# Optimization experiments

Measured on AMD Instinct MI355X. Metric: run time of the kernel, lower is better.

The kernel has to match this reference:

```python
import jax, jax.numpy as jnp
import numpy as np

EPS = 1e-5

def conv2d(x, w, stride=1, pad=0, groups=1):
    return jax.lax.conv_general_dilated(
        x, w, (stride, stride), [(pad, pad), (pad, pad)],
        feature_group_count=groups,
        dimension_numbers=('NCHW', 'OIHW', 'NCHW'))

def prelu(x, a):
    return jnp.where(x > 0, x, a[None, :, None, None] * x)

def batchnorm(x, g, b):
    # training-mode BN: batch statistics over N,H,W (biased variance, as torch)
    m = jnp.mean(x, axis=(0, 2, 3), keepdims=True)
    v = jnp.var(x, axis=(0, 2, 3), keepdims=True)
    xhat = (x - m) * jax.lax.rsqrt(v + EPS)
    return xhat * g[None, :, None, None] + b[None, :, None, None]

def setup_inputs() -> dict:
    key = jax.random.key(0)
    ks = jax.random.split(key, 8)
    C_in, C_out, stride = 128, 256, 2
    x = jax.random.normal(ks[0], (32, C_in, 56, 56), dtype=jnp.float32)
    w1 = jax.random.normal(ks[1], (C_out, C_in, 1, 1), dtype=jnp.float32) * 0.05
    w_dw = jax.random.normal(ks[2], (C_out, 1, 3, 3), dtype=jnp.float32) * 0.1
    w3 = jax.random.normal(ks[3], (C_out, C_out, 1, 1), dtype=jnp.float32) * 0.05
    w_adj = jax.random.normal(ks[4], (C_out, C_in, 1, 1), dtype=jnp.float32) * 0.05
    a_init = jnp.full((C_out,), 0.25, dtype=jnp.float32)  # PReLU init
    ones = jnp.ones((C_out,), dtype=jnp.float32)
    zeros = jnp.zeros((C_out,), dtype=jnp.float32)
    return {
        'x': x,
        'w1': w1, 'a1': a_init, 'g1': ones, 'b1': zeros,
        'w_dw': w_dw, 'a2': a_init, 'g2': ones, 'b2': zeros,
        'w3': w3, 'a3': a_init, 'g3': ones, 'b3': zeros,
        'w_adj': w_adj,
    }

def reference(x, w1, a1, g1, b1, w_dw, a2, g2, b2, w3, a3, g3, b3, w_adj):
    stride, C_out = 2, w_dw.shape[0]
    residual = conv2d(x, w_adj, stride=stride)  # full-precision shortcut
    xs = jnp.sign(x)
    # binary 1x1 conv (sign(x) already signed; sign is idempotent)
    out = conv2d(jnp.sign(xs), jnp.sign(w1))
    out = batchnorm(prelu(out, a1), g1, b1)
    # binary depthwise 3x3, stride, pad 1
    out = conv2d(jnp.sign(out), jnp.sign(w_dw), stride=stride, pad=1, groups=C_out)
    out = batchnorm(prelu(out, a2), g2, b2)
    # binary 1x1 conv
    out = conv2d(jnp.sign(out), jnp.sign(w3))
    out = batchnorm(prelu(out, a3), g3, b3)
    return out + residual
```

## Files before the change

### kernel.cpp

```cpp
#include <hip/hip_runtime.h>
#include <stdint.h>

#define NB   32
#define CIN  128
#define COUT 256
#define HH   56
#define WW   56
#define S1   (HH*WW)
#define HO   28
#define WO   28
#define S2   (HO*WO)
#define NS1  (NB*S1)
#define NS2  (NB*S2)
#define TOT2 (NS2*COUT)
#define EPSV 1e-5f

constexpr size_t OFF_XBITS = 0;
constexpr size_t OFF_WB1   = OFF_XBITS + (size_t)NS1*8*4;
constexpr size_t OFF_WB3   = OFF_WB1 + 256*8*4;
constexpr size_t OFF_WDW   = OFF_WB3 + 256*16*4;
constexpr size_t OFF_ACC   = OFF_WDW + 4096;
constexpr size_t OFF_WBADJ = OFF_ACC + 3*256*4*sizeof(int);
constexpr size_t OFF_XG    = OFF_WBADJ + (size_t)COUT*CIN*2;
constexpr size_t OFF_OUT1  = OFF_XG + (size_t)NS2*CIN*2;
constexpr size_t OFF_OUT2  = OFF_OUT1 + (size_t)NS1*COUT;
constexpr size_t OFF_XB2   = OFF_OUT2 + (size_t)TOT2;
constexpr size_t OFF_OUT3  = OFF_XB2 + (size_t)NS2*16*4;

typedef __attribute__((ext_vector_type(8))) short bf16x8;
typedef __attribute__((ext_vector_type(4))) float f32x4;

__device__ __forceinline__ uint32_t f2bf(float v) {
  uint32_t u = __float_as_uint(v);
  return (u + 0x7fffu + ((u >> 16) & 1u)) >> 16;
}

__device__ __forceinline__ void bn_finalize(const int* __restrict__ acc4,
                                            float a, float g, float b, float inv_ns,
                                            float& sc, float& sh) {
  float ps = (float)acc4[0];
  float ng = (float)acc4[1];
  float pq = (float)acc4[2];
  float nq = (float)acc4[3];
  float mean = (ps + a*ng) * inv_ns;
  float ex2  = (pq + a*a*nq) * inv_ns;
  float var  = ex2 - mean*mean;
  float rs   = rsqrtf(var + EPSV);
  sc = rs * g;
  sh = b - mean * sc;
}

__global__ __launch_bounds__(256) void packx_kernel(
    const float* __restrict__ x, uint32_t* __restrict__ xbits,
    uint32_t* __restrict__ xg,
    const float* __restrict__ w1, const float* __restrict__ w3,
    const float* __restrict__ wdw, const float* __restrict__ wadj,
    uint32_t* __restrict__ wb1, uint32_t* __restrict__ wb3,
    int8_t* __restrict__ wdws, uint32_t* __restrict__ wbadj,
    int* __restrict__ accbase) {
  int wdx = blockIdx.y;
  if (wdx == 0 && blockIdx.x < 256 && threadIdx.x < 64) {
    int co = blockIdx.x;
    int l  = threadIdx.x;
    if (l < 12) {
      int set = l >> 2, k = l & 3;
      accbase[set*1024 + co*4 + k] = 0;
    }
    for (int h = 0; h < 2; ++h) {
      float v = w1[(size_t)co*CIN + h*64 + l];
      unsigned long long bp = __ballot(v > 0.f);
      unsigned long long bn = __ballot(v < 0.f);
      if (l == 0) {
        wb1[co*8 + 2*h    ] = (uint32_t)bp;
        wb1[co*8 + 2*h + 1] = (uint32_t)(bp >> 32);
        wb1[co*8 + 4 + 2*h    ] = (uint32_t)bn;
        wb1[co*8 + 4 + 2*h + 1] = (uint32_t)(bn >> 32);
      }
    }
    for (int h = 0; h < 4; ++h) {
      float v = w3[(size_t)co*COUT + h*64 + l];
      unsigned long long bp = __ballot(v > 0.f);
      unsigned long long bn = __ballot(v < 0.f);
      if (l == 0) {
        wb3[co*16 + 2*h    ] = (uint32_t)bp;
        wb3[co*16 + 2*h + 1] = (uint32_t)(bp >> 32);
        wb3[co*16 + 8 + 2*h    ] = (uint32_t)bn;
        wb3[co*16 + 8 + 2*h + 1] = (uint32_t)(bn >> 32);
      }
    }
    if (l < 9) {
      float v = wdw[co*9 + l];
      wdws[co*9 + l] = (int8_t)((v > 0.f) - (v < 0.f));
    }
    {
      float v0 = wadj[(size_t)co*CIN + 2*l];
      float v1 = wadj[(size_t)co*CIN + 2*l + 1];
      wbadj[co*64 + l] = f2bf(v0) | (f2bf(v1) << 16);
    }
  }

  int m = blockIdx.x*256 + threadIdx.x;
  int n = m / S1, hw = m % S1;
  size_t base = ((size_t)n*CIN + wdx*32)*S1 + hw;
  uint32_t p = 0, q = 0;
  uint32_t bv[16];
  #pragma unroll
  for (int j = 0; j < 32; ++j) {
    float v = x[base + (size_t)j*S1];
    p |= (uint32_t)(v > 0.f) << j;
    q |= (uint32_t)(v < 0.f) << j;
    uint32_t b = f2bf(v);
    if (j & 1) bv[j >> 1] |= b << 16; else bv[j >> 1] = b;
  }
  xbits[(size_t)m*8 + wdx    ] = p;
  xbits[(size_t)m*8 + 4 + wdx] = q;
  int h = hw / WW, w = hw % WW;
  if (((h | w) & 1) == 0) {
    int m2 = n*S2 + (h >> 1)*WO + (w >> 1);
    uint4* dst = (uint4*)(xg + (size_t)m2*64 + wdx*16);
    dst[0] = make_uint4(bv[0],  bv[1],  bv[2],  bv[3]);
    dst[1] = make_uint4(bv[4],  bv[5],  bv[6],  bv[7]);
    dst[2] = make_uint4(bv[8],  bv[9],  bv[10], bv[11]);
    dst[3] = make_uint4(bv[12], bv[13], bv[14], bv[15]);
  }
}

__global__ __launch_bounds__(256) void conv1_kernel(
    const uint32_t* __restrict__ xb, const uint32_t* __restrict__ wb,
    int8_t* __restrict__ out1, int* __restrict__ accum1) {
  int tid = threadIdx.x;
  int qm = blockIdx.x*256 + tid;
  int m0 = qm*8;
  int n  = m0 / S1;
  int hw0 = m0 - n*S1;
  int co0 = blockIdx.y * 8;

  const uint4* xw = (const uint4*)(xb + (size_t)m0*8);
  uint4 xp0 = xw[0],  xq0 = xw[1];
  uint4 xp1 = xw[2],  xq1 = xw[3];
  uint4 xp2 = xw[4],  xq2 = xw[5];
  uint4 xp3 = xw[6],  xq3 = xw[7];
  uint4 xp4 = xw[8],  xq4 = xw[9];
  uint4 xp5 = xw[10], xq5 = xw[11];
  uint4 xp6 = xw[12], xq6 = xw[13];
  uint4 xp7 = xw[14], xq7 = xw[15];

#define NZP(i) ((xp##i.x|xq##i.x)&(xp##i.y|xq##i.y)&(xp##i.z|xq##i.z)&(xp##i.w|xq##i.w))
  bool allnz = ((NZP(0)&NZP(1)&NZP(2)&NZP(3)&NZP(4)&NZP(5)&NZP(6)&NZP(7)) == 0xffffffffu);
#undef NZP

  __shared__ int sl[256][33];
  uint32_t rA[8], rB[8];

  #pragma unroll
  for (int j = 0; j < 8; ++j) {
    const uint32_t* w8 = wb + (size_t)(co0 + j)*8;
    uint32_t w0 = w8[0], w1 = w8[1], w2 = w8[2], w3 = w8[3];
    int A0,A1,A2,A3,A4,A5,A6,A7;
#define XORDOT(i,A) A = 128 - 2*(__popc(xp##i.x^w0)+__popc(xp##i.y^w1)+__popc(xp##i.z^w2)+__popc(xp##i.w^w3));
    XORDOT(0,A0) XORDOT(1,A1) XORDOT(2,A2) XORDOT(3,A3)
    XORDOT(4,A4) XORDOT(5,A5) XORDOT(6,A6) XORDOT(7,A7)
#undef XORDOT
    if (!allnz) {
#define ZCORR(i,A) { \
      uint32_t z0 = ~(xp##i.x|xq##i.x), z1 = ~(xp##i.y|xq##i.y); \
      uint32_t z2 = ~(xp##i.z|xq##i.z), z3 = ~(xp##i.w|xq##i.w); \
      A += 2*(__popc(z0&w0)+__popc(z1&w1)+__popc(z2&w2)+__popc(z3&w3)) \
         - (__popc(z0)+__popc(z1)+__popc(z2)+__popc(z3)); }
      ZCORR(0,A0) ZCORR(1,A1) ZCORR(2,A2) ZCORR(3,A3)
      ZCORR(4,A4) ZCORR(5,A5) ZCORR(6,A6) ZCORR(7,A7)
#undef ZCORR
    }
    if (A0 > 127) A0 = 127;
    if (A1 > 127) A1 = 127;
    if (A2 > 127) A2 = 127;
    if (A3 > 127) A3 = 127;
    if (A4 > 127) A4 = 127;
    if (A5 > 127) A5 = 127;
    if (A6 > 127) A6 = 127;
    if (A7 > 127) A7 = 127;
    rA[j] = (uint32_t)(uint8_t)A0 | ((uint32_t)(uint8_t)A1 << 8)
          | ((uint32_t)(uint8_t)A2 << 16) | ((uint32_t)(uint8_t)A3 << 24);
    rB[j] = (uint32_t)(uint8_t)A4 | ((uint32_t)(uint8_t)A5 << 8)
          | ((uint32_t)(uint8_t)A6 << 16) | ((uint32_t)(uint8_t)A7 << 24);
    int ps = 0, ns = 0, pq = 0, nq = 0;
#define STAT(A) if (A > 0) { ps += A; pq += A*A; } else { ns += A; nq += A*A; }
    STAT(A0) STAT(A1) STAT(A2) STAT(A3) STAT(A4) STAT(A5) STAT(A6) STAT(A7)
#undef STAT
    sl[tid][j*4+0] = ps; sl[tid][j*4+1] = ns;
    sl[tid][j*4+2] = pq; sl[tid][j*4+3] = nq;
  }
  __syncthreads();

  #pragma unroll
  for (int j = 0; j < 8; ++j) {
    uint32_t* dst = (uint32_t*)(out1 + (size_t)(n*COUT + co0 + j)*S1 + hw0);
    dst[0] = rA[j];
    dst[1] = rB[j];
  }

  int s = tid & 31, g = tid >> 5;
  int part = 0;
  #pragma unroll
  for (int i = 0; i < 32; ++i) part += sl[g*32 + i][s];
  part += __shfl_xor(part, 32);
  __shared__ int sW[4][32];
  if ((tid & 63) < 32) sW[tid >> 6][s] = part;
  __syncthreads();
  if (tid < 32) {
    int tot = sW[0][tid] + sW[1][tid] + sW[2][tid] + sW[3][tid];
    atomicAdd(&accum1[co0*4 + tid], tot);
  }
}

#define DW_SLABS 8
#define DW_RB    68
__global__ __launch_bounds__(256) void dw_kernel(
    const int8_t* __restrict__ out1, const int8_t* __restrict__ wdws,
    const int* __restrict__ acc1, const float* __restrict__ a1,
    const float* __restrict__ g1, const float* __restrict__ b1,
    int8_t* __restrict__ out2, int* __restrict__ accum2) {
  __shared__ int8_t sl[DW_SLABS][57][DW_RB];
  __shared__ int sTp[DW_SLABS], sTn[DW_SLABS], sAcc[DW_SLABS][4];
  int tid = threadIdx.x;
  int nc0 = blockIdx.x * DW_SLABS;
  int co0 = nc0 & (COUT-1);

  int* slw = (int*)&sl[0][0][0];
  #pragma unroll
  for (int i = tid; i < DW_SLABS*57*DW_RB/4; i += 256) slw[i] = 0;
  if (tid < DW_SLABS) { sTp[tid] = 128; sTn[tid] = -129; }
  if (tid < DW_SLABS*4) sAcc[tid >> 2][tid & 3] = 0;
  __syncthreads();

  {
    int slab = tid >> 5;
    int co = co0 + slab;
    float av = a1[co], sc, sh;
    bn_finalize(acc1 + co*4, av, g1[co], b1[co], 1.f/NS1, sc, sh);
    int tp = 128, tn = -129;
    int v0 = -128 + (tid & 31)*8;
    #pragma unroll
    for (int k = 0; k < 8; ++k) {
      int v = v0 + k;
      float f = (float)v;
      float pr = f > 0.f ? f : av*f;
      float tv = pr*sc + sh;
      if (tv > 0.f && v < tp) tp = v;
      if (tv < 0.f && v > tn) tn = v;
    }
    atomicMin(&sTp[slab], tp);
    atomicMax(&sTn[slab], tn);
  }
  __syncthreads();

  for (int i = tid; i < DW_SLABS*784; i += 256) {
    int slab = i / 784;
    int d    = i - slab*784;
    int ih   = d / 14;
    int iwd  = d - ih*14;
    int Tp = sTp[slab], Tn = sTn[slab];
    uint32_t v4 = ((const uint32_t*)(out1 + (size_t)(nc0 + slab)*S1))[d];
    uint32_t s4 = 0;
    #pragma unroll
    for (int k = 0; k < 4; ++k) {
      int v = (int)(int8_t)(v4 >> (8*k));
      int s = (v >= Tp) - (v <= Tn);
      s4 |= (uint32_t)(s & 0xff) << (8*k);
    }
    *(uint32_t*)&sl[slab][ih + 1][4 + 4*iwd] = s4;
  }
  __syncthreads();

  int psum = 0, nsum = 0, psq = 0, nsq = 0;
  int slabD = tid / HO;
  if (tid < DW_SLABS*HO) {
    int ho   = tid - slabD*HO;
    int nc = nc0 + slabD;
    int co = co0 + slabD;
    int wv[9];
    #pragma unroll
    for (int k = 0; k < 9; ++k) wv[k] = wdws[co*9 + k];
    const uint32_t* r0 = (const uint32_t*)&sl[slabD][2*ho    ][4];
    const uint32_t* r1 = (const uint32_t*)&sl[slabD][2*ho + 1][4];
    const uint32_t* r2 = (const uint32_t*)&sl[slabD][2*ho + 2][4];
    uint32_t* o32 = (uint32_t*)(out2 + (size_t)nc*S2 + ho*WO);
    int c0 = 0, c1 = 0, c2 = 0;
    uint32_t obuf = 0;
    #pragma unroll
    for (int q = 0; q < 14; ++q) {
      uint32_t d0 = r0[q], d1 = r1[q], d2 = r2[q];
      int s00=(int)(int8_t)d0, s01=(int)(int8_t)(d0>>8), s02=(int)(int8_t)(d0>>16), s03=(int)(int8_t)(d0>>24);
      int s10=(int)(int8_t)d1, s11=(int)(int8_t)(d1>>8), s12=(int)(int8_t)(d1>>16), s13=(int)(int8_t)(d1>>24);
      int s20=(int)(int8_t)d2, s21=(int)(int8_t)(d2>>8), s22=(int)(int8_t)(d2>>16), s23=(int)(int8_t)(d2>>24);
      int a0 = c0*wv[0] + s00*wv[1] + s01*wv[2]
             + c1*wv[3] + s10*wv[4] + s11*wv[5]
             + c2*wv[6] + s20*wv[7] + s21*wv[8];
      int a1v = s01*wv[0] + s02*wv[1] + s03*wv[2]
              + s11*wv[3] + s12*wv[4] + s13*wv[5]
              + s21*wv[6] + s22*wv[7] + s23*wv[8];
      c0 = s03; c1 = s13; c2 = s23;
      if (a0 > 0) { psum += a0; psq += a0*a0; } else { nsum += a0; nsq += a0*a0; }
      if (a1v > 0) { psum += a1v; psq += a1v*a1v; } else { nsum += a1v; nsq += a1v*a1v; }
      if ((q & 1) == 0) {
        obuf = (uint32_t)(a0 & 0xff) | ((uint32_t)(a1v & 0xff) << 8);
      } else {
        obuf |= ((uint32_t)(a0 & 0xff) << 16) | ((uint32_t)(a1v & 0xff) << 24);
        o32[q >> 1] = obuf;
      }
    }
    atomicAdd(&sAcc[slabD][0], psum);
    atomicAdd(&sAcc[slabD][1], nsum);
    atomicAdd(&sAcc[slabD][2], psq);
    atomicAdd(&sAcc[slabD][3], nsq);
  }
  __syncthreads();

  if (tid < DW_SLABS*4) {
    int slab = tid >> 2, k = tid & 3;
    atomicAdd(&accum2[(co0 + slab)*4 + k], sAcc[slab][k]);
  }
}

__global__ __launch_bounds__(256) void pack2_kernel(
    const int8_t* __restrict__ out2, const int* __restrict__ acc2,
    const float* __restrict__ a2, const float* __restrict__ g2,
    const float* __restrict__ b2, uint32_t* __restrict__ xb2) {
  __shared__ int sTp[32], sTn[32];
  int wdx = blockIdx.y;
  if (threadIdx.x < 32) {
    int c = wdx*32 + threadIdx.x;
    float av = a2[c], sc, sh;
    bn_finalize(acc2 + c*4, av, g2[c], b2[c], 1.f/NS2, sc, sh);
    int tp = 10, tn = -10;
    for (int v = -9; v <= 9; ++v) {
      float f = (float)v;
      float pr = f > 0.f ? f : av*f;
      float tv = pr*sc + sh;
      if (tv > 0.f && v < tp) tp = v;
      if (tv < 0.f && v > tn) tn = v;
    }
    sTp[threadIdx.x] = tp; sTn[threadIdx.x] = tn;
  }
  __syncthreads();
  int m = blockIdx.x*256 + threadIdx.x;
  int n = m / S2, hw = m % S2;
  uint32_t p = 0, q = 0;
  #pragma unroll
  for (int j = 0; j < 32; ++j) {
    int c = wdx*32 + j;
    int v = out2[(size_t)(n*COUT + c)*S2 + hw];
    p |= (uint32_t)(v >= sTp[j]) << j;
    q |= (uint32_t)(v <= sTn[j]) << j;
  }
  xb2[(size_t)m*16 + wdx    ] = p;
  xb2[(size_t)m*16 + 8 + wdx] = q;
}

__global__ __launch_bounds__(256) void conv3_kernel(
    const uint32_t* __restrict__ xb2, const uint32_t* __restrict__ wb3,
    int16_t* __restrict__ out3, int* __restrict__ accum3) {
  int tid = threadIdx.x;
  int qm = blockIdx.x*256 + tid;
  int m0 = qm*2;
  int n  = m0 / S2;
  int hw0 = m0 - n*S2;
  int co0 = blockIdx.y * 8;

  const uint4* xw = (const uint4*)(xb2 + (size_t)m0*16);
  uint4 P0a = xw[0], P0b = xw[1], Q0a = xw[2], Q0b = xw[3];
  uint4 P1a = xw[4], P1b = xw[5], Q1a = xw[6], Q1b = xw[7];

  uint32_t nz = (P0a.x|Q0a.x)&(P0a.y|Q0a.y)&(P0a.z|Q0a.z)&(P0a.w|Q0a.w)
              & (P0b.x|Q0b.x)&(P0b.y|Q0b.y)&(P0b.z|Q0b.z)&(P0b.w|Q0b.w)
              & (P1a.x|Q1a.x)&(P1a.y|Q1a.y)&(P1a.z|Q1a.z)&(P1a.w|Q1a.w)
              & (P1b.x|Q1b.x)&(P1b.y|Q1b.y)&(P1b.z|Q1b.z)&(P1b.w|Q1b.w);

  uint32_t res[8];
  if (nz == 0xffffffffu) {
    #pragma unroll
    for (int j = 0; j < 8; ++j) {
      const uint32_t* w = wb3 + (size_t)(co0 + j)*16;
      int s0 = __popc(P0a.x^w[0])+__popc(P0a.y^w[1])+__popc(P0a.z^w[2])+__popc(P0a.w^w[3])
             + __popc(P0b.x^w[4])+__popc(P0b.y^w[5])+__popc(P0b.z^w[6])+__popc(P0b.w^w[7]);
      int s1 = __popc(P1a.x^w[0])+__popc(P1a.y^w[1])+__popc(P1a.z^w[2])+__popc(P1a.w^w[3])
             + __popc(P1b.x^w[4])+__popc(P1b.y^w[5])+__popc(P1b.z^w[6])+__popc(P1b.w^w[7]);
      int a0 = 256 - 2*s0, a1 = 256 - 2*s1;
      res[j] = (uint32_t)(uint16_t)(int16_t)a0 | ((uint32_t)(uint16_t)(int16_t)a1 << 16);
    }
  } else {
    #pragma unroll
    for (int j = 0; j < 8; ++j) {
      const uint32_t* w = wb3 + (size_t)(co0 + j)*16;
      int a0 = __popc(P0a.x&w[0])+__popc(P0a.y&w[1])+__popc(P0a.z&w[2])+__popc(P0a.w&w[3])
             + __popc(P0b.x&w[4])+__popc(P0b.y&w[5])+__popc(P0b.z&w[6])+__popc(P0b.w&w[7])
             + __popc(Q0a.x&w[8])+__popc(Q0a.y&w[9])+__popc(Q0a.z&w[10])+__popc(Q0a.w&w[11])
             + __popc(Q0b.x&w[12])+__popc(Q0b.y&w[13])+__popc(Q0b.z&w[14])+__popc(Q0b.w&w[15])
             - __popc(P0a.x&w[8])-__popc(P0a.y&w[9])-__popc(P0a.z&w[10])-__popc(P0a.w&w[11])
             - __popc(P0b.x&w[12])-__popc(P0b.y&w[13])-__popc(P0b.z&w[14])-__popc(P0b.w&w[15])
             - __popc(Q0a.x&w[0])-__popc(Q0a.y&w[1])-__popc(Q0a.z&w[2])-__popc(Q0a.w&w[3])
             - __popc(Q0b.x&w[4])-__popc(Q0b.y&w[5])-__popc(Q0b.z&w[6])-__popc(Q0b.w&w[7]);
      int a1 = __popc(P1a.x&w[0])+__popc(P1a.y&w[1])+__popc(P1a.z&w[2])+__popc(P1a.w&w[3])
             + __popc(P1b.x&w[4])+__popc(P1b.y&w[5])+__popc(P1b.z&w[6])+__popc(P1b.w&w[7])
             + __popc(Q1a.x&w[8])+__popc(Q1a.y&w[9])+__popc(Q1a.z&w[10])+__popc(Q1a.w&w[11])
             + __popc(Q1b.x&w[12])+__popc(Q1b.y&w[13])+__popc(Q1b.z&w[14])+__popc(Q1b.w&w[15])
             - __popc(P1a.x&w[8])-__popc(P1a.y&w[9])-__popc(P1a.z&w[10])-__popc(P1a.w&w[11])
             - __popc(P1b.x&w[12])-__popc(P1b.y&w[13])-__popc(P1b.z&w[14])-__popc(P1b.w&w[15])
             - __popc(Q1a.x&w[0])-__popc(Q1a.y&w[1])-__popc(Q1a.z&w[2])-__popc(Q1a.w&w[3])
             - __popc(Q1b.x&w[4])-__popc(Q1b.y&w[5])-__popc(Q1b.z&w[6])-__popc(Q1b.w&w[7]);
      res[j] = (uint32_t)(uint16_t)(int16_t)a0 | ((uint32_t)(uint16_t)(int16_t)a1 << 16);
    }
  }

  __shared__ int sl[256][33];
  #pragma unroll
  for (int j = 0; j < 8; ++j) {
    int b0 = (int)(int16_t)(res[j] & 0xffff);
    int b1 = (int)(int16_t)(res[j] >> 16);
    int ps = 0, ns = 0, pq = 0, nq = 0;
    if (b0 > 0) { ps += b0; pq += b0*b0; } else { ns += b0; nq += b0*b0; }
    if (b1 > 0) { ps += b1; pq += b1*b1; } else { ns += b1; nq += b1*b1; }
    sl[tid][j*4+0] = ps; sl[tid][j*4+1] = ns;
    sl[tid][j*4+2] = pq; sl[tid][j*4+3] = nq;
  }
  __syncthreads();

  #pragma unroll
  for (int j = 0; j < 8; ++j)
    *(uint32_t*)(out3 + (size_t)(n*COUT + co0 + j)*S2 + hw0) = res[j];

  int s = tid & 31, g = tid >> 5;
  int part = 0;
  #pragma unroll
  for (int i = 0; i < 32; ++i) part += sl[g*32 + i][s];
  part += __shfl_xor(part, 32);
  __shared__ int sW[4][32];
  if ((tid & 63) < 32) sW[tid >> 6][s] = part;
  __syncthreads();
  if (tid < 32) {
    int tot = sW[0][tid] + sW[1][tid] + sW[2][tid] + sW[3][tid];
    atomicAdd(&accum3[co0*4 + tid], tot);
  }
}

__global__ __launch_bounds__(256) void resfinal_kernel(
    const uint16_t* __restrict__ xg, const uint16_t* __restrict__ wb,
    const int16_t* __restrict__ out3,
    const float* __restrict__ a3, const float* __restrict__ g3,
    const float* __restrict__ b3, const int* __restrict__ acc3,
    float* __restrict__ out) {
  int lane = threadIdx.x & 63;
  int wid  = threadIdx.x >> 6;
  int m0  = blockIdx.x*64 + wid*16;
  int r16 = lane & 15, hi = lane >> 4;
  int koff = hi * 8;

  const bf16x8* arow = (const bf16x8*)(xg + (size_t)(m0 + r16)*CIN + koff);
  bf16x8 af0 = arow[0], af1 = arow[4], af2 = arow[8], af3 = arow[12];

  f32x4 dd[16];
  #pragma unroll
  for (int t = 0; t < 16; ++t) {
    const bf16x8* brow = (const bf16x8*)(wb + (size_t)(t*16 + r16)*CIN + koff);
    f32x4 a = {0.f,0.f,0.f,0.f};
    a = __builtin_amdgcn_mfma_f32_16x16x32_bf16(af0, brow[0],  a, 0,0,0);
    a = __builtin_amdgcn_mfma_f32_16x16x32_bf16(af1, brow[4],  a, 0,0,0);
    a = __builtin_amdgcn_mfma_f32_16x16x32_bf16(af2, brow[8],  a, 0,0,0);
    a = __builtin_amdgcn_mfma_f32_16x16x32_bf16(af3, brow[12], a, 0,0,0);
    dd[t] = a;
  }

  int mrow = m0 + hi*4;
  int n  = mrow / S2;
  int hw = mrow - n*S2;
  #pragma unroll
  for (int t = 0; t < 16; ++t) {
    int co = t*16 + r16;
    float av = a3[co], sc, sh;
    bn_finalize(acc3 + co*4, av, g3[co], b3[co], 1.f/NS2, sc, sh);
    size_t o = ((size_t)n*COUT + co)*S2 + hw;
    #pragma unroll
    for (int r = 0; r < 4; ++r) {
      float f = (float)out3[o + r];
      float pp = f > 0.f ? f : av*f;
      out[o + r] = pp*sc + sh + dd[t][r];
    }
  }
}

extern "C" void kernel_launch(void* const* d_in, const int* in_sizes, int n_in,
                              void* d_out, int out_size, void* d_ws, size_t ws_size,
                              hipStream_t stream) {
  (void)in_sizes; (void)n_in; (void)out_size; (void)ws_size;
  const float* x    = (const float*)d_in[0];
  const float* w1   = (const float*)d_in[1];
  const float* a1   = (const float*)d_in[2];
  const float* g1   = (const float*)d_in[3];
  const float* b1   = (const float*)d_in[4];
  const float* wdw  = (const float*)d_in[5];
  const float* a2   = (const float*)d_in[6];
  const float* g2   = (const float*)d_in[7];
  const float* b2   = (const float*)d_in[8];
  const float* w3   = (const float*)d_in[9];
  const float* a3   = (const float*)d_in[10];
  const float* g3   = (const float*)d_in[11];
  const float* b3   = (const float*)d_in[12];
  const float* wadj = (const float*)d_in[13];
  float* out = (float*)d_out;

  char* ws = (char*)d_ws;
  uint32_t* xbits = (uint32_t*)(ws + OFF_XBITS);
  uint32_t* wb1   = (uint32_t*)(ws + OFF_WB1);
  uint32_t* wb3   = (uint32_t*)(ws + OFF_WB3);
  int8_t*   wdws  = (int8_t*)  (ws + OFF_WDW);
  int*      acc1  = (int*)     (ws + OFF_ACC);
  int*      acc2  = acc1 + 256*4;
  int*      acc3  = acc2 + 256*4;
  uint32_t* wbadj = (uint32_t*)(ws + OFF_WBADJ);
  uint32_t* xg    = (uint32_t*)(ws + OFF_XG);
  int8_t*   out1  = (int8_t*)  (ws + OFF_OUT1);
  int8_t*   out2  = (int8_t*)  (ws + OFF_OUT2);
  uint32_t* xb2   = (uint32_t*)(ws + OFF_XB2);
  int16_t*  out3  = (int16_t*) (ws + OFF_OUT3);

  packx_kernel<<<dim3(NS1/256, 4), 256, 0, stream>>>(
      x, xbits, xg, w1, w3, wdw, wadj, wb1, wb3, wdws, wbadj, acc1);
  conv1_kernel<<<dim3(NS1/2048, 32), 256, 0, stream>>>(xbits, wb1, out1, acc1);
  dw_kernel<<<NB*COUT/DW_SLABS, 256, 0, stream>>>(out1, wdws, acc1, a1, g1, b1, out2, acc2);
  pack2_kernel<<<dim3(NS2/256, 8), 256, 0, stream>>>(out2, acc2, a2, g2, b2, xb2);
  conv3_kernel<<<dim3(NS2/512, 32), 256, 0, stream>>>(xb2, wb3, out3, acc3);
  resfinal_kernel<<<NS2/64, 256, 0, stream>>>(
      (const uint16_t*)xg, (const uint16_t*)wbadj, out3, a3, g3, b3, acc3, out);
}
```

Before: 112.6 us.

## Halve conv1 per-thread pixels and reshape stat reduction to avoid bank conflicts

The conv1 kernel now processes 4 pixels per thread instead of 8, doubling the grid so more blocks are in flight and per-thread register use drops. The per-block statistic reduction is split into two 16-column passes over a narrower shared array, with strided row access and an extra shuffle. The conv3 reduction switches to strided row indexing, likely to reduce LDS bank conflicts. In exchange there are more blocks, twice as many atomics per block group, and extra barriers.

```diff
diff --git a/kernel.cpp b/kernel.cpp
--- a/kernel.cpp
+++ b/kernel.cpp
@@ -130,36 +130,35 @@
     int8_t* __restrict__ out1, int* __restrict__ accum1) {
   int tid = threadIdx.x;
   int qm = blockIdx.x*256 + tid;
-  int m0 = qm*8;
+  int m0 = qm*4;
   int n  = m0 / S1;
   int hw0 = m0 - n*S1;
   int co0 = blockIdx.y * 8;
 
   const uint4* xw = (const uint4*)(xb + (size_t)m0*8);
-  uint4 xp0 = xw[0],  xq0 = xw[1];
-  uint4 xp1 = xw[2],  xq1 = xw[3];
-  uint4 xp2 = xw[4],  xq2 = xw[5];
-  uint4 xp3 = xw[6],  xq3 = xw[7];
-  uint4 xp4 = xw[8],  xq4 = xw[9];
-  uint4 xp5 = xw[10], xq5 = xw[11];
-  uint4 xp6 = xw[12], xq6 = xw[13];
-  uint4 xp7 = xw[14], xq7 = xw[15];
-
-#define NZP(i) ((xp##i.x|xq##i.x)&(xp##i.y|xq##i.y)&(xp##i.z|xq##i.z)&(xp##i.w|xq##i.w))
-  bool allnz = ((NZP(0)&NZP(1)&NZP(2)&NZP(3)&NZP(4)&NZP(5)&NZP(6)&NZP(7)) == 0xffffffffu);
-#undef NZP
-
-  __shared__ int sl[256][33];
-  uint32_t rA[8], rB[8];
+  uint4 xp0 = xw[0], xq0 = xw[1];
+  uint4 xp1 = xw[2], xq1 = xw[3];
+  uint4 xp2 = xw[4], xq2 = xw[5];
+  uint4 xp3 = xw[6], xq3 = xw[7];
+
+  uint32_t nzw = (xp0.x|xq0.x)&(xp0.y|xq0.y)&(xp0.z|xq0.z)&(xp0.w|xq0.w)
+               & (xp1.x|xq1.x)&(xp1.y|xq1.y)&(xp1.z|xq1.z)&(xp1.w|xq1.w)
+               & (xp2.x|xq2.x)&(xp2.y|xq2.y)&(xp2.z|xq2.z)&(xp2.w|xq2.w)
+               & (xp3.x|xq3.x)&(xp3.y|xq3.y)&(xp3.z|xq3.z)&(xp3.w|xq3.w);
+  bool allnz = (nzw == 0xffffffffu);
+
+  __shared__ int sl[256][17];
+  __shared__ int sW[4][16];
+  uint32_t res[8];
+  int stp[8], stn[8], stpq[8], stnq[8];
 
   #pragma unroll
   for (int j = 0; j < 8; ++j) {
     const uint32_t* w8 = wb + (size_t)(co0 + j)*8;
     uint32_t w0 = w8[0], w1 = w8[1], w2 = w8[2], w3 = w8[3];
-    int A0,A1,A2,A3,A4,A5,A6,A7;
+    int A0,A1,A2,A3;
 #define XORDOT(i,A) A = 128 - 2*(__popc(xp##i.x^w0)+__popc(xp##i.y^w1)+__popc(xp##i.z^w2)+__popc(xp##i.w^w3));
     XORDOT(0,A0) XORDOT(1,A1) XORDOT(2,A2) XORDOT(3,A3)
-    XORDOT(4,A4) XORDOT(5,A5) XORDOT(6,A6) XORDOT(7,A7)
 #undef XORDOT
     if (!allnz) {
 #define ZCORR(i,A) { \
@@ -168,48 +167,65 @@
       A += 2*(__popc(z0&w0)+__popc(z1&w1)+__popc(z2&w2)+__popc(z3&w3)) \
          - (__popc(z0)+__popc(z1)+__popc(z2)+__popc(z3)); }
       ZCORR(0,A0) ZCORR(1,A1) ZCORR(2,A2) ZCORR(3,A3)
-      ZCORR(4,A4) ZCORR(5,A5) ZCORR(6,A6) ZCORR(7,A7)
 #undef ZCORR
     }
     if (A0 > 127) A0 = 127;
     if (A1 > 127) A1 = 127;
     if (A2 > 127) A2 = 127;
     if (A3 > 127) A3 = 127;
-    if (A4 > 127) A4 = 127;
-    if (A5 > 127) A5 = 127;
-    if (A6 > 127) A6 = 127;
-    if (A7 > 127) A7 = 127;
-    rA[j] = (uint32_t)(uint8_t)A0 | ((uint32_t)(uint8_t)A1 << 8)
-          | ((uint32_t)(uint8_t)A2 << 16) | ((uint32_t)(uint8_t)A3 << 24);
-    rB[j] = (uint32_t)(uint8_t)A4 | ((uint32_t)(uint8_t)A5 << 8)
-          | ((uint32_t)(uint8_t)A6 << 16) | ((uint32_t)(uint8_t)A7 << 24);
+    res[j] = (uint32_t)(uint8_t)A0 | ((uint32_t)(uint8_t)A1 << 8)
+           | ((uint32_t)(uint8_t)A2 << 16) | ((uint32_t)(uint8_t)A3 << 24);
     int ps = 0, ns = 0, pq = 0, nq = 0;
 #define STAT(A) if (A > 0) { ps += A; pq += A*A; } else { ns += A; nq += A*A; }
-    STAT(A0) STAT(A1) STAT(A2) STAT(A3) STAT(A4) STAT(A5) STAT(A6) STAT(A7)
+    STAT(A0) STAT(A1) STAT(A2) STAT(A3)
 #undef STAT
-    sl[tid][j*4+0] = ps; sl[tid][j*4+1] = ns;
-    sl[tid][j*4+2] = pq; sl[tid][j*4+3] = nq;
-  }
-  __syncthreads();
-
-  #pragma unroll
-  for (int j = 0; j < 8; ++j) {
-    uint32_t* dst = (uint32_t*)(out1 + (size_t)(n*COUT + co0 + j)*S1 + hw0);
-    dst[0] = rA[j];
-    dst[1] = rB[j];
-  }
-
-  int s = tid & 31, g = tid >> 5;
-  int part = 0;
-  #pragma unroll
-  for (int i = 0; i < 32; ++i) part += sl[g*32 + i][s];
-  part += __shfl_xor(part, 32);
-  __shared__ int sW[4][32];
-  if ((tid & 63) < 32) sW[tid >> 6][s] = part;
-  __syncthreads();
-  if (tid < 32) {
+    stp[j] = ps; stn[j] = ns; stpq[j] = pq; stnq[j] = nq;
+  }
+
+  #pragma unroll
+  for (int j = 0; j < 4; ++j) {
+    sl[tid][j*4+0] = stp[j];  sl[tid][j*4+1] = stn[j];
+    sl[tid][j*4+2] = stpq[j]; sl[tid][j*4+3] = stnq[j];
+  }
+  __syncthreads();
+
+  #pragma unroll
+  for (int j = 0; j < 8; ++j)
+    *(uint32_t*)(out1 + (size_t)(n*COUT + co0 + j)*S1 + hw0) = res[j];
+
+  int s16 = tid & 15, ch = tid >> 4;
+  {
+    int part = 0;
+    #pragma unroll
+    for (int i = 0; i < 16; ++i) part += sl[ch + 16*i][s16];
+    part += __shfl_xor(part, 16);
+    part += __shfl_xor(part, 32);
+    if ((tid & 63) < 16) sW[tid >> 6][s16] = part;
+  }
+  __syncthreads();
+  if (tid < 16) {
     int tot = sW[0][tid] + sW[1][tid] + sW[2][tid] + sW[3][tid];
     atomicAdd(&accum1[co0*4 + tid], tot);
+  }
+
+  #pragma unroll
+  for (int j = 0; j < 4; ++j) {
+    sl[tid][j*4+0] = stp[4+j];  sl[tid][j*4+1] = stn[4+j];
+    sl[tid][j*4+2] = stpq[4+j]; sl[tid][j*4+3] = stnq[4+j];
+  }
+  __syncthreads();
+  {
+    int part = 0;
+    #pragma unroll
+    for (int i = 0; i < 16; ++i) part += sl[ch + 16*i][s16];
+    part += __shfl_xor(part, 16);
+    part += __shfl_xor(part, 32);
+    if ((tid & 63) < 16) sW[tid >> 6][s16] = part;
+  }
+  __syncthreads();
+  if (tid < 16) {
+    int tot = sW[0][tid] + sW[1][tid] + sW[2][tid] + sW[3][tid];
+    atomicAdd(&accum1[co0*4 + 16 + tid], tot);
   }
 }
 
@@ -432,7 +448,7 @@
   int s = tid & 31, g = tid >> 5;
   int part = 0;
   #pragma unroll
-  for (int i = 0; i < 32; ++i) part += sl[g*32 + i][s];
+  for (int i = 0; i < 32; ++i) part += sl[g + 8*i][s];
   part += __shfl_xor(part, 32);
   __shared__ int sW[4][32];
   if ((tid & 63) < 32) sW[tid >> 6][s] = part;
@@ -525,7 +541,7 @@
 
   packx_kernel<<<dim3(NS1/256, 4), 256, 0, stream>>>(
       x, xbits, xg, w1, w3, wdw, wadj, wb1, wb3, wdws, wbadj, acc1);
-  conv1_kernel<<<dim3(NS1/2048, 32), 256, 0, stream>>>(xbits, wb1, out1, acc1);
+  conv1_kernel<<<dim3(NS1/1024, 32), 256, 0, stream>>>(xbits, wb1, out1, acc1);
   dw_kernel<<<NB*COUT/DW_SLABS, 256, 0, stream>>>(out1, wdws, acc1, a1, g1, b1, out2, acc2);
   pack2_kernel<<<dim3(NS2/256, 8), 256, 0, stream>>>(out2, acc2, a2, g2, b2, xb2);
   conv3_kernel<<<dim3(NS2/512, 32), 256, 0, stream>>>(xb2, wb3, out3, acc3);
```

Measured after the change: 110.6 us. About the same (-1.8%).
